# Kernel optimization log

Hardware: AMD Instinct MI355X
Metric: run time of the kernel (lower is better)

The kernel has to match this reference:

```python
import jax, jax.numpy as jnp
import numpy as np

B, V, C = 4, 50000, 160


def rotation_6d_to_matrix(d6):
    """pytorch3d-style 6D rotation -> 3x3 matrix (rows b1,b2,b3)."""
    a1, a2 = d6[..., :3], d6[..., 3:]
    eps = 1e-8
    b1 = a1 / jnp.maximum(jnp.linalg.norm(a1, axis=-1, keepdims=True), eps)
    a2p = a2 - jnp.sum(b1 * a2, axis=-1, keepdims=True) * b1
    b2 = a2p / jnp.maximum(jnp.linalg.norm(a2p, axis=-1, keepdims=True), eps)
    b3 = jnp.cross(b1, b2)
    return jnp.stack([b1, b2, b3], axis=-2)  # (..., 3, 3)


def setup_inputs() -> dict:
    key = jax.random.key(0)
    k1, k2, k3, k4, k5 = jax.random.split(key, 5)
    X = jax.random.normal(k1, (B, V, 3), dtype=jnp.float32)
    V_nodes = jax.random.normal(k2, (B, C, 3), dtype=jnp.float32) * 0.1
    rot6d_nodes = jax.random.normal(k3, (B, C, 6), dtype=jnp.float32)
    W_nodes = jax.random.uniform(k4, (V, C), dtype=jnp.float32)
    W_nodes = W_nodes / jnp.sum(W_nodes, axis=1, keepdims=True)  # row-normalized skinning weights
    idx_nn_to_nodes = jax.random.randint(k5, (C,), 0, V, dtype=jnp.int64)
    return {"X": X, "V_nodes": V_nodes, "rot6d_nodes": rot6d_nodes,
            "W_nodes": W_nodes, "idx_nn_to_nodes": idx_nn_to_nodes}


def reference(X, V_nodes, rot6d_nodes, W_nodes, idx_nn_to_nodes):
    # R: (B, C, 3, 3)
    R = rotation_6d_to_matrix(rot6d_nodes)
    # gather node centers: (B, C, 3)
    center = X[:, idx_nn_to_nodes, :]
    # disp: (B, V, C, 3)
    disp = X[:, :, None, :] - center[:, None, :, :]
    # rotate displacement by per-node rotation, add back center + node offset
    Rdisp = jnp.einsum('bvcd,bckd->bvck', disp, R) \
            + center[:, None, :, :] + V_nodes[:, None, :, :]  # (B, V, C, 3)
    # weighted skinning sum over nodes: (B, V, 3)
    out = jnp.einsum('vc,bvck->bvk', W_nodes, Rdisp)
    return out
```

## Files before the change

### kernel.cpp

```cpp
#include <hip/hip_runtime.h>

#define Bv 4
#define Vv 50000
#define Cv 160

__global__ void precompute_A(const float* __restrict__ X,
                             const float* __restrict__ Vn,
                             const float* __restrict__ r6,
                             const int* __restrict__ idx,
                             float* __restrict__ A) {
    int i = blockIdx.x * blockDim.x + threadIdx.x;
    if (i >= Bv * Cv) return;
    int b = i / Cv, c = i % Cv;

    const float* d6 = r6 + (size_t)(b * Cv + c) * 6;
    float a1x = d6[0], a1y = d6[1], a1z = d6[2];
    float a2x = d6[3], a2y = d6[4], a2z = d6[5];

    float n1 = fmaxf(sqrtf(a1x*a1x + a1y*a1y + a1z*a1z), 1e-8f);
    float b1x = a1x / n1, b1y = a1y / n1, b1z = a1z / n1;

    float d = b1x*a2x + b1y*a2y + b1z*a2z;
    float px = a2x - d*b1x, py = a2y - d*b1y, pz = a2z - d*b1z;
    float n2 = fmaxf(sqrtf(px*px + py*py + pz*pz), 1e-8f);
    float b2x = px / n2, b2y = py / n2, b2z = pz / n2;

    float b3x = b1y*b2z - b1z*b2y;
    float b3y = b1z*b2x - b1x*b2z;
    float b3z = b1x*b2y - b1y*b2x;

    int iv = idx[c];
    const float* xc = X + ((size_t)b * Vv + iv) * 3;
    float cx = xc[0], cy = xc[1], cz = xc[2];
    const float* vn = Vn + (size_t)(b * Cv + c) * 3;
    float vx = vn[0], vy = vn[1], vz = vn[2];

    float* Ao = A + (size_t)(b * Cv + c) * 12;
    Ao[0] = b1x; Ao[1] = b1y; Ao[2] = b1z;
    Ao[3] = b2x; Ao[4] = b2y; Ao[5] = b2z;
    Ao[6] = b3x; Ao[7] = b3y; Ao[8] = b3z;
    Ao[9]  = cx + vx - (b1x*cx + b1y*cy + b1z*cz);
    Ao[10] = cy + vy - (b2x*cx + b2y*cy + b2z*cz);
    Ao[11] = cz + vz - (b3x*cx + b3y*cy + b3z*cz);
}

__global__ __launch_bounds__(512) void deform_main(const float* __restrict__ X,
                                                   const float* __restrict__ W,
                                                   const float* __restrict__ A,
                                                   float* __restrict__ out) {
    __shared__ float P[4 * 64 * 13];

    const int tid  = threadIdx.x;
    const int lane = tid & 63;
    const int wv   = __builtin_amdgcn_readfirstlane(tid >> 6);
    const int b    = wv & 3;
    const int half = wv >> 2;
    const int v0   = blockIdx.x * 64;
    const int v    = v0 + lane;
    const bool valid = (v < Vv);
    const int vc   = valid ? v : (Vv - 1);

    const float4* __restrict__ Wrow =
        (const float4*)(W + (size_t)vc * Cv) + half * 20;
    const float* __restrict__ Ab = A + ((size_t)b * Cv + (size_t)half * 80) * 12;

    float acc[12];
#pragma unroll
    for (int j = 0; j < 12; ++j) acc[j] = 0.0f;

#pragma unroll 2
    for (int c4 = 0; c4 < 20; ++c4) {
        float4 wq = Wrow[c4];
        const float wj[4] = {wq.x, wq.y, wq.z, wq.w};
#pragma unroll
        for (int j = 0; j < 4; ++j) {
            const float* a = Ab + (size_t)(c4 * 4 + j) * 12;
            float w = wj[j];
#pragma unroll
            for (int k = 0; k < 12; ++k) acc[k] = fmaf(w, a[k], acc[k]);
        }
    }

    if (half) {
        float* p = &P[(b * 64 + lane) * 13];
#pragma unroll
        for (int j = 0; j < 12; ++j) p[j] = acc[j];
    }
    __syncthreads();

    if (!half) {
        const float* p = &P[(b * 64 + lane) * 13];
#pragma unroll
        for (int j = 0; j < 12; ++j) acc[j] += p[j];

        if (valid) {
            const float* xp = X + ((size_t)b * Vv + v) * 3;
            float x0 = xp[0], x1 = xp[1], x2 = xp[2];
            float o0 = acc[0]*x0 + acc[1]*x1 + acc[2]*x2 + acc[9];
            float o1 = acc[3]*x0 + acc[4]*x1 + acc[5]*x2 + acc[10];
            float o2 = acc[6]*x0 + acc[7]*x1 + acc[8]*x2 + acc[11];
            float* op = out + ((size_t)b * Vv + v) * 3;
            op[0] = o0; op[1] = o1; op[2] = o2;
        }
    }
}

extern "C" void kernel_launch(void* const* d_in, const int* in_sizes, int n_in,
                              void* d_out, int out_size, void* d_ws, size_t ws_size,
                              hipStream_t stream) {
    const float* X   = (const float*)d_in[0];
    const float* Vn  = (const float*)d_in[1];
    const float* r6  = (const float*)d_in[2];
    const float* W   = (const float*)d_in[3];
    const int*   idx = (const int*)d_in[4];
    float* out = (float*)d_out;
    float* A = (float*)d_ws;

    precompute_A<<<(Bv * Cv + 255) / 256, 256, 0, stream>>>(X, Vn, r6, idx, A);
    deform_main<<<(Vv + 63) / 64, 512, 0, stream>>>(X, W, A, out);
}
```

Before: 100.1 us.

## Transpose skinning weights into column-major workspace for coalesced per-node loads

Adds a separate kernel that transposes W (V x C) into a padded C x VPAD layout in the workspace via a shared-memory tile. The main kernel then reads one weight per node per lane with contiguous addresses across the wavefront, replacing per-lane strided float4 row reads. This costs an extra full read and write of W (about 32 MB each) and an extra launch on every call. The aim is more coalesced loads in the main loop, which may not pay for the added traffic.

```diff
diff --git a/kernel.cpp b/kernel.cpp
--- a/kernel.cpp
+++ b/kernel.cpp
@@ -3,6 +3,8 @@
 #define Bv 4
 #define Vv 50000
 #define Cv 160
+#define TILES 782
+#define VPAD  50048
 
 __global__ void precompute_A(const float* __restrict__ X,
                              const float* __restrict__ Vn,
@@ -44,8 +46,35 @@
     Ao[11] = cz + vz - (b3x*cx + b3y*cy + b3z*cz);
 }
 
+__global__ __launch_bounds__(256) void transpose_W(const float* __restrict__ W,
+                                                   float* __restrict__ WT) {
+    __shared__ float T[64 * 165];
+    const int tid = threadIdx.x;
+    const int v0  = blockIdx.x * 64;
+
+    for (int i = tid; i < 64 * 40; i += 256) {
+        int r = i / 40, c4 = i % 40;
+        int row = v0 + r;
+        if (row >= Vv) row = Vv - 1;
+        float4 q = ((const float4*)(W + (size_t)row * Cv))[c4];
+        float* t = &T[r * 165 + c4 * 4];
+        t[0] = q.x; t[1] = q.y; t[2] = q.z; t[3] = q.w;
+    }
+    __syncthreads();
+
+    for (int i = tid; i < Cv * 16; i += 256) {
+        int c = i / 16, g = i % 16;
+        float4 q;
+        q.x = T[(g * 4 + 0) * 165 + c];
+        q.y = T[(g * 4 + 1) * 165 + c];
+        q.z = T[(g * 4 + 2) * 165 + c];
+        q.w = T[(g * 4 + 3) * 165 + c];
+        ((float4*)(WT + (size_t)c * VPAD + v0))[g] = q;
+    }
+}
+
 __global__ __launch_bounds__(512) void deform_main(const float* __restrict__ X,
-                                                   const float* __restrict__ W,
+                                                   const float* __restrict__ WT,
                                                    const float* __restrict__ A,
                                                    float* __restrict__ out) {
     __shared__ float P[4 * 64 * 13];
@@ -58,10 +87,8 @@
     const int v0   = blockIdx.x * 64;
     const int v    = v0 + lane;
     const bool valid = (v < Vv);
-    const int vc   = valid ? v : (Vv - 1);
 
-    const float4* __restrict__ Wrow =
-        (const float4*)(W + (size_t)vc * Cv) + half * 20;
+    const float* __restrict__ Wcol = WT + (size_t)(half * 80) * VPAD + v0 + lane;
     const float* __restrict__ Ab = A + ((size_t)b * Cv + (size_t)half * 80) * 12;
 
     float acc[12];
@@ -70,12 +97,11 @@
 
 #pragma unroll 2
     for (int c4 = 0; c4 < 20; ++c4) {
-        float4 wq = Wrow[c4];
-        const float wj[4] = {wq.x, wq.y, wq.z, wq.w};
 #pragma unroll
         for (int j = 0; j < 4; ++j) {
-            const float* a = Ab + (size_t)(c4 * 4 + j) * 12;
-            float w = wj[j];
+            int c = c4 * 4 + j;
+            float w = Wcol[(size_t)c * VPAD];
+            const float* a = Ab + (size_t)c * 12;
 #pragma unroll
             for (int k = 0; k < 12; ++k) acc[k] = fmaf(w, a[k], acc[k]);
         }
@@ -88,20 +114,18 @@
     }
     __syncthreads();
 
-    if (!half) {
+    if (!half && valid) {
         const float* p = &P[(b * 64 + lane) * 13];
 #pragma unroll
         for (int j = 0; j < 12; ++j) acc[j] += p[j];
 
-        if (valid) {
-            const float* xp = X + ((size_t)b * Vv + v) * 3;
-            float x0 = xp[0], x1 = xp[1], x2 = xp[2];
-            float o0 = acc[0]*x0 + acc[1]*x1 + acc[2]*x2 + acc[9];
-            float o1 = acc[3]*x0 + acc[4]*x1 + acc[5]*x2 + acc[10];
-            float o2 = acc[6]*x0 + acc[7]*x1 + acc[8]*x2 + acc[11];
-            float* op = out + ((size_t)b * Vv + v) * 3;
-            op[0] = o0; op[1] = o1; op[2] = o2;
-        }
+        const float* xp = X + ((size_t)b * Vv + v) * 3;
+        float x0 = xp[0], x1 = xp[1], x2 = xp[2];
+        float o0 = acc[0]*x0 + acc[1]*x1 + acc[2]*x2 + acc[9];
+        float o1 = acc[3]*x0 + acc[4]*x1 + acc[5]*x2 + acc[10];
+        float o2 = acc[6]*x0 + acc[7]*x1 + acc[8]*x2 + acc[11];
+        float* op = out + ((size_t)b * Vv + v) * 3;
+        op[0] = o0; op[1] = o1; op[2] = o2;
     }
 }
 
@@ -114,8 +138,11 @@
     const float* W   = (const float*)d_in[3];
     const int*   idx = (const int*)d_in[4];
     float* out = (float*)d_out;
-    float* A = (float*)d_ws;
+
+    float* A  = (float*)d_ws;
+    float* WT = (float*)((char*)d_ws + 32768);
 
     precompute_A<<<(Bv * Cv + 255) / 256, 256, 0, stream>>>(X, Vn, r6, idx, A);
-    deform_main<<<(Vv + 63) / 64, 512, 0, stream>>>(X, W, A, out);
+    transpose_W<<<TILES, 256, 0, stream>>>(W, WT);
+    deform_main<<<TILES, 512, 0, stream>>>(X, WT, A, out);
 }
```

Measured after the change: 113.6 us. +13.4%, slower.
